# Kernel tuning notes

Hardware: AMD Instinct MI355X
Metric: run time of the kernel (lower is better)

Reference implementation:

```python
import jax, jax.numpy as jnp
import numpy as np

N_USERS = 4096
N_ITEMS = 4096
D = 64
L = 2
B = 4096
N = N_USERS + N_ITEMS


def setup_inputs() -> dict:
    key = jax.random.key(0)
    ks = jax.random.split(key, 24)
    g = lambda i, shape: jax.random.normal(ks[i], shape, dtype=jnp.float32) * 0.05
    # sparse-ish 0/1 adjacency (module calls adj.to_dense(); ~16 neighbors/node)
    adj = (jax.random.uniform(ks[0], (N, N), dtype=jnp.float32) < 0.002).astype(jnp.float32)
    users = jax.random.randint(ks[1], (B,), 0, N_USERS)
    pos_items = jax.random.randint(ks[2], (B,), 0, N_ITEMS)
    neg_items = jax.random.randint(ks[3], (B,), 0, N_ITEMS)
    return {
        "adj_matrix": adj,
        "users": users,
        "pos_items": pos_items,
        "neg_items": neg_items,
        "user_table": g(4, (N_USERS, D)),
        "item_table": g(5, (N_ITEMS, D)),
        "gcn_W": g(6, (L, D, D)), "gcn_b": g(7, (L, D)),
        "gat_W": g(8, (L, D, D)), "gat_b": g(9, (L, D)),
        "attn_W": g(10, (L, 2 * D)), "attn_b": g(11, (L,)),
        "fuse_W": g(12, (L, 2 * D, D)), "fuse_b": g(13, (L, D)),
        "actor_W": g(14, (D, D)), "actor_b": g(15, (D,)),
        "critic_W1": g(16, (2 * D, D)), "critic_b1": g(17, (D,)),
        "critic_W2": g(18, (D, 1)), "critic_b2": g(19, (1,)),
        "layer_weights": jnp.ones((L,), dtype=jnp.float32),
    }


def _leaky(x):
    return jnp.where(x >= 0, x, 0.01 * x)  # F.leaky_relu default slope


def reference(adj_matrix, users, pos_items, neg_items, user_table, item_table,
              gcn_W, gcn_b, gat_W, gat_b, attn_W, attn_b, fuse_W, fuse_b,
              actor_W, actor_b, critic_W1, critic_b1, critic_W2, critic_b2,
              layer_weights):
    all_emb = jnp.concatenate([user_table, item_table], axis=0)  # [N, D]

    # GCN stack: spmm(adj, x) then linear, relu
    gcn = [all_emb]
    for l in range(L):
        h = adj_matrix @ gcn[-1]
        gcn.append(jax.nn.relu(h @ gcn_W[l] + gcn_b[l]))

    # GAT stack: e[i,j] = leaky_relu(a1.h_i + a2.h_j + b); multiply-mask by adj, row softmax
    gat = [all_emb]
    for l in range(L):
        h = gat[-1] @ gat_W[l] + gat_b[l]  # [N, D]
        a1, a2 = attn_W[l, :D], attn_W[l, D:]
        e = _leaky((h @ a1)[:, None] + (h @ a2)[None, :] + attn_b[l])  # [N, N]
        attn = jax.nn.softmax(e * adj_matrix, axis=1)  # faithful: multiply-mask, not -inf
        gat.append(jax.nn.relu(attn @ h))

    lw = jax.nn.softmax(layer_weights)
    fused = jnp.zeros((N, D), dtype=all_emb.dtype)
    for i in range(L):
        cat = jnp.concatenate([gcn[i + 1], gat[i + 1]], axis=1)  # [N, 2D]
        fused = fused + lw[i] * jax.nn.relu(cat @ fuse_W[i] + fuse_b[i])

    user_emb, item_emb = fused[:N_USERS], fused[N_USERS:]
    u = user_emb[users]
    p = item_emb[pos_items]
    n = item_emb[neg_items]

    uf = u @ actor_W + actor_b  # Actor
    pos_score = jnp.sum(uf * p, axis=1)
    neg_score = jnp.sum(uf * n, axis=1)

    def critic(a, b):
        x = jnp.concatenate([a, b], axis=1)
        hidden = jax.nn.relu(x @ critic_W1 + critic_b1)
        return hidden @ critic_W2 + critic_b2

    return pos_score, neg_score, critic(u, p), critic(u, n)
```

## Files before the change

### kernel.cpp

```cpp
#include <hip/hip_runtime.h>

#define NTOT 8192
#define NU 4096
#define D 64
#define MAXN 64
#define ND (NTOT*D)

typedef float f4 __attribute__((ext_vector_type(4)));

__device__ __forceinline__ float wsum(float x){
  #pragma unroll
  for(int o=32;o;o>>=1) x += __shfl_xor(x,o);
  return x;
}
__device__ __forceinline__ float wmax(float x){
  #pragma unroll
  for(int o=32;o;o>>=1) x = fmaxf(x,__shfl_xor(x,o));
  return x;
}
__device__ __forceinline__ float bcastf(float x, int k){
  return __uint_as_float(__builtin_amdgcn_readlane(__float_as_uint(x),(unsigned)k));
}
__device__ __forceinline__ int bcasti(int x, int k){
  return (int)__builtin_amdgcn_readlane((unsigned)x,(unsigned)k);
}

__global__ __launch_bounds__(256) void kA(const float* __restrict__ adj,
    const float* __restrict__ ut, const float* __restrict__ it,
    const float* __restrict__ gat_W, const float* __restrict__ gat_b,
    const float* __restrict__ attn_W,
    float* __restrict__ all_emb, float* __restrict__ h0,
    float* __restrict__ q0v, float* __restrict__ k0v, float* __restrict__ S0,
    int* __restrict__ ell, int* __restrict__ nnz){
  __shared__ float Ws[D*D];
  __shared__ float red[4][D];
  int tid = threadIdx.x, lane = tid & 63, wid = tid >> 6;
  int row = blockIdx.x*4 + wid;
  for(int i = tid; i < D*D; i += 256) Ws[i] = gat_W[i];

  float x = (row < NU) ? ut[row*D + lane] : it[(row-NU)*D + lane];
  all_emb[row*D + lane] = x;

  const f4* arow = (const f4*)(adj + (size_t)row * NTOT);
  unsigned nibs[4] = {0u,0u,0u,0u};
  #pragma unroll 4
  for(int ch = 0; ch < 32; ++ch){
    f4 v = arow[ch*64 + lane];
    unsigned nib = (v.x!=0.f?1u:0u) | (v.y!=0.f?2u:0u) | (v.z!=0.f?4u:0u) | (v.w!=0.f?8u:0u);
    nibs[ch>>3] |= nib << ((ch&7)*4);
  }

  int base = 0;
  #pragma unroll
  for(int g = 0; g < 4; ++g){
    unsigned ng = nibs[g];
    for(int s = 0; s < 8; ++s){
      unsigned nib = (ng >> (s*4)) & 0xFu;
      if(__ballot(nib != 0u) == 0ull) continue;
      int ch = g*8 + s;
      #pragma unroll
      for(int j = 0; j < 4; ++j){
        unsigned long long m = __ballot(((nib>>j)&1u) != 0u);
        if(m){
          if((nib>>j)&1u){
            int below = __builtin_amdgcn_mbcnt_hi((unsigned)(m>>32),
                        __builtin_amdgcn_mbcnt_lo((unsigned)m, 0u));
            int slot = base + below;
            if(slot < MAXN) ell[row*MAXN + slot] = (ch*64 + lane)*4 + j;
          }
          base += __popcll(m);
        }
      }
    }
  }
  int cnt = base > MAXN ? MAXN : base;
  if(lane == 0) nnz[row] = cnt;

  __syncthreads();
  float h = gat_b[lane];
  #pragma unroll 16
  for(int k = 0; k < D; ++k) h = fmaf(bcastf(x, k), Ws[k*D + lane], h);
  h0[row*D + lane] = h;
  float q  = wsum(h * attn_W[lane]);
  float kk = wsum(h * attn_W[D + lane]);
  if(lane == 0){ q0v[row] = q; k0v[row] = kk; }
  red[wid][lane] = h;
  __syncthreads();
  if(wid == 0)
    atomicAdd(&S0[lane], red[0][lane] + red[1][lane] + red[2][lane] + red[3][lane]);
}

__global__ __launch_bounds__(256) void kB(
    const float* __restrict__ all_emb, const float* __restrict__ h0,
    const float* __restrict__ q0v, const float* __restrict__ k0v, const float* __restrict__ S0,
    const int* __restrict__ ell, const int* __restrict__ nnz,
    const float* __restrict__ gcn_W, const float* __restrict__ gcn_b,
    const float* __restrict__ gat_W, const float* __restrict__ gat_b,
    const float* __restrict__ attn_W, const float* __restrict__ attn_b,
    const float* __restrict__ fuse_W, const float* __restrict__ fuse_b,
    const float* __restrict__ layer_w,
    float* __restrict__ gcn1, float* __restrict__ fusedb, float* __restrict__ h1,
    float* __restrict__ q1v, float* __restrict__ k1v, float* __restrict__ S1){
  __shared__ float Ws[D*D];
  __shared__ float red[4][D];
  int tid = threadIdx.x, lane = tid & 63, wid = tid >> 6;
  int row = blockIdx.x*4 + wid;
  int cnt = nnz[row];
  int mycol = ell[row*MAXN + lane];

  for(int i = tid; i < D*D; i += 256) Ws[i] = gcn_W[i];

  float q  = q0v[row];
  float ab = attn_b[0];
  int colg = (lane < cnt) ? mycol : 0;
  float e = -1e30f;
  if(lane < cnt){
    float xx = q + k0v[colg] + ab;
    e = (xx >= 0.f) ? xx : 0.01f * xx;
  }
  float m  = fmaxf(0.f, wmax(e));
  float w  = (lane < cnt) ? expf(e - m) : 0.f;
  float em = expf(-m);
  float Z  = (float)(NTOT - cnt) * em + wsum(w);

  float accg = 0.f, acca = 0.f, hs = 0.f;
  int tt = 0;
  for(; tt + 4 <= cnt; tt += 4){
    int c0 = bcasti(mycol, tt),   c1 = bcasti(mycol, tt+1);
    int c2 = bcasti(mycol, tt+2), c3 = bcasti(mycol, tt+3);
    float w0 = bcastf(w, tt),   w1 = bcastf(w, tt+1);
    float w2 = bcastf(w, tt+2), w3 = bcastf(w, tt+3);
    float e0 = all_emb[c0*D + lane], e1 = all_emb[c1*D + lane];
    float e2 = all_emb[c2*D + lane], e3 = all_emb[c3*D + lane];
    float h0v = h0[c0*D + lane], h1v = h0[c1*D + lane];
    float h2v = h0[c2*D + lane], h3v = h0[c3*D + lane];
    accg += (e0 + e1) + (e2 + e3);
    acca = fmaf(w0, h0v, fmaf(w1, h1v, fmaf(w2, h2v, fmaf(w3, h3v, acca))));
    hs   += (h0v + h1v) + (h2v + h3v);
  }
  for(; tt < cnt; ++tt){
    int   c  = bcasti(mycol, tt);
    float wt = bcastf(w, tt);
    float ev = all_emb[c*D + lane];
    float hv = h0[c*D + lane];
    accg += ev;
    acca  = fmaf(wt, hv, acca);
    hs   += hv;
  }
  float g1 = fmaxf((acca + em*(S0[lane] - hs)) / Z, 0.f);

  __syncthreads();
  float yg = gcn_b[lane];
  #pragma unroll 16
  for(int k = 0; k < D; ++k) yg = fmaf(bcastf(accg, k), Ws[k*D + lane], yg);
  float gc1 = fmaxf(yg, 0.f);
  gcn1[row*D + lane] = gc1;
  __syncthreads();

  float l0 = layer_w[0], l1 = layer_w[1];
  float mx = fmaxf(l0, l1);
  float ex0 = expf(l0 - mx), ex1 = expf(l1 - mx);
  float lw0 = ex0 / (ex0 + ex1);
  for(int i = tid; i < D*D; i += 256) Ws[i] = fuse_W[i];
  __syncthreads();
  float y = fuse_b[lane];
  #pragma unroll 16
  for(int k = 0; k < D; ++k) y = fmaf(bcastf(gc1, k), Ws[k*D + lane], y);
  __syncthreads();
  for(int i = tid; i < D*D; i += 256) Ws[i] = fuse_W[D*D + i];
  __syncthreads();
  #pragma unroll 16
  for(int k = 0; k < D; ++k) y = fmaf(bcastf(g1, k), Ws[k*D + lane], y);
  fusedb[row*D + lane] = lw0 * fmaxf(y, 0.f);
  __syncthreads();

  for(int i = tid; i < D*D; i += 256) Ws[i] = gat_W[D*D + i];
  __syncthreads();
  float h = gat_b[D + lane];
  #pragma unroll 16
  for(int k = 0; k < D; ++k) h = fmaf(bcastf(g1, k), Ws[k*D + lane], h);
  h1[row*D + lane] = h;
  float qq = wsum(h * attn_W[2*D + lane]);
  float kk = wsum(h * attn_W[3*D + lane]);
  if(lane == 0){ q1v[row] = qq; k1v[row] = kk; }
  red[wid][lane] = h;
  __syncthreads();
  if(wid == 0)
    atomicAdd(&S1[lane], red[0][lane] + red[1][lane] + red[2][lane] + red[3][lane]);
}

__global__ __launch_bounds__(256) void kC(
    const int* __restrict__ ell, const int* __restrict__ nnz,
    const float* __restrict__ gcn1, const float* __restrict__ h1,
    const float* __restrict__ q1v, const float* __restrict__ k1v, const float* __restrict__ S1,
    const float* __restrict__ gcn_W, const float* __restrict__ gcn_b,
    const float* __restrict__ attn_b,
    const float* __restrict__ fuse_W, const float* __restrict__ fuse_b,
    const float* __restrict__ layer_w,
    float* __restrict__ fusedb){
  __shared__ float Ws[D*D];
  int tid = threadIdx.x, lane = tid & 63, wid = tid >> 6;
  int row = blockIdx.x*4 + wid;
  int cnt = nnz[row];
  int mycol = ell[row*MAXN + lane];

  for(int i = tid; i < D*D; i += 256) Ws[i] = gcn_W[D*D + i];

  float q  = q1v[row];
  float ab = attn_b[1];
  int colg = (lane < cnt) ? mycol : 0;
  float e = -1e30f;
  if(lane < cnt){
    float xx = q + k1v[colg] + ab;
    e = (xx >= 0.f) ? xx : 0.01f * xx;
  }
  float m  = fmaxf(0.f, wmax(e));
  float w  = (lane < cnt) ? expf(e - m) : 0.f;
  float em = expf(-m);
  float Z  = (float)(NTOT - cnt) * em + wsum(w);

  float accg = 0.f, acca = 0.f, hs = 0.f;
  int tt = 0;
  for(; tt + 4 <= cnt; tt += 4){
    int c0 = bcasti(mycol, tt),   c1 = bcasti(mycol, tt+1);
    int c2 = bcasti(mycol, tt+2), c3 = bcasti(mycol, tt+3);
    float w0 = bcastf(w, tt),   w1 = bcastf(w, tt+1);
    float w2 = bcastf(w, tt+2), w3 = bcastf(w, tt+3);
    float g0 = gcn1[c0*D + lane], g1_ = gcn1[c1*D + lane];
    float g2_ = gcn1[c2*D + lane], g3 = gcn1[c3*D + lane];
    float h0v = h1[c0*D + lane], h1v = h1[c1*D + lane];
    float h2v = h1[c2*D + lane], h3v = h1[c3*D + lane];
    accg += (g0 + g1_) + (g2_ + g3);
    acca = fmaf(w0, h0v, fmaf(w1, h1v, fmaf(w2, h2v, fmaf(w3, h3v, acca))));
    hs   += (h0v + h1v) + (h2v + h3v);
  }
  for(; tt < cnt; ++tt){
    int   c  = bcasti(mycol, tt);
    float wt = bcastf(w, tt);
    float gv = gcn1[c*D + lane];
    float hv = h1[c*D + lane];
    accg += gv;
    acca  = fmaf(wt, hv, acca);
    hs   += hv;
  }
  float g2 = fmaxf((acca + em*(S1[lane] - hs)) / Z, 0.f);

  __syncthreads();
  float yg = gcn_b[D + lane];
  #pragma unroll 16
  for(int k = 0; k < D; ++k) yg = fmaf(bcastf(accg, k), Ws[k*D + lane], yg);
  float gc2 = fmaxf(yg, 0.f);
  __syncthreads();

  float l0 = layer_w[0], l1 = layer_w[1];
  float mx = fmaxf(l0, l1);
  float ex0 = expf(l0 - mx), ex1 = expf(l1 - mx);
  float lw1 = ex1 / (ex0 + ex1);
  for(int i = tid; i < D*D; i += 256) Ws[i] = fuse_W[2*D*D + i];
  __syncthreads();
  float y = fuse_b[D + lane];
  #pragma unroll 16
  for(int k = 0; k < D; ++k) y = fmaf(bcastf(gc2, k), Ws[k*D + lane], y);
  __syncthreads();
  for(int i = tid; i < D*D; i += 256) Ws[i] = fuse_W[3*D*D + i];
  __syncthreads();
  #pragma unroll 16
  for(int k = 0; k < D; ++k) y = fmaf(bcastf(g2, k), Ws[k*D + lane], y);
  fusedb[row*D + lane] += lw1 * fmaxf(y, 0.f);
}

__global__ __launch_bounds__(256) void kD(const float* __restrict__ fused,
    const int* __restrict__ users, const int* __restrict__ pos, const int* __restrict__ neg,
    const float* __restrict__ AW, const float* __restrict__ abias,
    const float* __restrict__ cW1, const float* __restrict__ cb1,
    const float* __restrict__ cW2, const float* __restrict__ cb2,
    float* __restrict__ out){
  __shared__ float AWs[D*D];
  __shared__ float C1s[2*D*D];
  __shared__ float abs_[D], cb1s[D], C2s[D];
  int tid = threadIdx.x;
  for(int i = tid; i < D*D; i += 256) AWs[i] = AW[i];
  for(int i = tid; i < 2*D*D; i += 256) C1s[i] = cW1[i];
  if(tid < D){
    abs_[tid] = abias[tid];
    cb1s[tid] = cb1[tid];
    C2s[tid]  = cW2[tid];
  }
  __syncthreads();
  int lane = tid & 63;
  int bi   = blockIdx.x*4 + (tid >> 6);
  int ui = users[bi], pi = pos[bi] + NU, ni = neg[bi] + NU;
  float ud = fused[ui*D + lane], pd = fused[pi*D + lane], nd = fused[ni*D + lane];
  float ufd = abs_[lane];
  #pragma unroll 16
  for(int k = 0; k < D; ++k) ufd = fmaf(bcastf(ud, k), AWs[k*D + lane], ufd);
  float ps = wsum(ufd * pd);
  float ns = wsum(ufd * nd);
  float hu = cb1s[lane];
  #pragma unroll 16
  for(int k = 0; k < D; ++k) hu = fmaf(bcastf(ud, k), C1s[k*D + lane], hu);
  float hp = hu, hn = hu;
  #pragma unroll 16
  for(int k = 0; k < D; ++k){
    float pk = bcastf(pd, k), nk = bcastf(nd, k);
    hp = fmaf(pk, C1s[(D+k)*D + lane], hp);
    hn = fmaf(nk, C1s[(D+k)*D + lane], hn);
  }
  hp = fmaxf(hp, 0.f); hn = fmaxf(hn, 0.f);
  float cp = wsum(hp * C2s[lane]);
  float cn = wsum(hn * C2s[lane]);
  if(lane == 0){
    out[bi]         = ps;
    out[4096  + bi] = ns;
    out[8192  + bi] = cp + cb2[0];
    out[12288 + bi] = cn + cb2[0];
  }
}

extern "C" void kernel_launch(void* const* d_in, const int* in_sizes, int n_in,
                              void* d_out, int out_size, void* d_ws, size_t ws_size,
                              hipStream_t stream){
  const float* adj        = (const float*)d_in[0];
  const int*   users      = (const int*)d_in[1];
  const int*   pos        = (const int*)d_in[2];
  const int*   neg        = (const int*)d_in[3];
  const float* user_table = (const float*)d_in[4];
  const float* item_table = (const float*)d_in[5];
  const float* gcn_W      = (const float*)d_in[6];
  const float* gcn_b      = (const float*)d_in[7];
  const float* gat_W      = (const float*)d_in[8];
  const float* gat_b      = (const float*)d_in[9];
  const float* attn_W     = (const float*)d_in[10];
  const float* attn_b     = (const float*)d_in[11];
  const float* fuse_W     = (const float*)d_in[12];
  const float* fuse_b     = (const float*)d_in[13];
  const float* actor_W    = (const float*)d_in[14];
  const float* actor_b    = (const float*)d_in[15];
  const float* cW1        = (const float*)d_in[16];
  const float* cb1        = (const float*)d_in[17];
  const float* cW2        = (const float*)d_in[18];
  const float* cb2        = (const float*)d_in[19];
  const float* layer_w    = (const float*)d_in[20];

  float* ws      = (float*)d_ws;
  float* all_emb = ws;
  float* h0      = all_emb + ND;
  float* h1      = h0 + ND;
  float* gcn1    = h1 + ND;
  float* fusedb  = gcn1 + ND;
  float* q0v     = fusedb + ND;
  float* k0v     = q0v + NTOT;
  float* q1v     = k0v + NTOT;
  float* k1v     = q1v + NTOT;
  float* S0      = k1v + NTOT;
  float* S1      = S0 + D;
  int*   nnz     = (int*)(S1 + D);
  int*   ell     = nnz + NTOT;

  hipMemsetAsync(S0, 0, 2*D*sizeof(float), stream);
  kA<<<NTOT/4, 256, 0, stream>>>(adj, user_table, item_table, gat_W, gat_b, attn_W,
                                 all_emb, h0, q0v, k0v, S0, ell, nnz);
  kB<<<NTOT/4, 256, 0, stream>>>(all_emb, h0, q0v, k0v, S0, ell, nnz,
                                 gcn_W, gcn_b, gat_W, gat_b, attn_W, attn_b,
                                 fuse_W, fuse_b, layer_w,
                                 gcn1, fusedb, h1, q1v, k1v, S1);
  kC<<<NTOT/4, 256, 0, stream>>>(ell, nnz, gcn1, h1, q1v, k1v, S1,
                                 gcn_W, gcn_b, attn_b, fuse_W, fuse_b, layer_w,
                                 fusedb);
  kD<<<1024, 256, 0, stream>>>(fusedb, users, pos, neg, actor_W, actor_b,
                               cW1, cb1, cW2, cb2, (float*)d_out);
}
```

Baseline: 199.4 us.

## Split adjacency scan into separate kernel with one block per row

```diff
diff --git a/kernel.cpp b/kernel.cpp
--- a/kernel.cpp
+++ b/kernel.cpp
@@ -25,57 +25,69 @@
   return (int)__builtin_amdgcn_readlane((unsigned)x,(unsigned)k);
 }
 
-__global__ __launch_bounds__(256) void kA(const float* __restrict__ adj,
-    const float* __restrict__ ut, const float* __restrict__ it,
+__global__ __launch_bounds__(256) void kScan(const float* __restrict__ adj,
+                                             int* __restrict__ ell, int* __restrict__ nnz){
+  __shared__ int cbuf[4][MAXN];
+  __shared__ int wcnt[4];
+  int tid = threadIdx.x, lane = tid & 63, wid = tid >> 6;
+  int row = blockIdx.x;
+  const f4* arow = (const f4*)(adj + (size_t)row * NTOT);
+
+  unsigned nibsw = 0u;
+  #pragma unroll
+  for(int ch = 0; ch < 8; ++ch){
+    f4 v = arow[ch*256 + tid];
+    unsigned nib = (v.x!=0.f?1u:0u) | (v.y!=0.f?2u:0u) | (v.z!=0.f?4u:0u) | (v.w!=0.f?8u:0u);
+    nibsw |= nib << (ch*4);
+  }
+
+  int base = 0;
+  #pragma unroll
+  for(int ch = 0; ch < 8; ++ch){
+    unsigned nib = (nibsw >> (ch*4)) & 0xFu;
+    if(__ballot(nib != 0u) == 0ull) continue;
+    int f4idx = ch*256 + wid*64;
+    #pragma unroll
+    for(int j = 0; j < 4; ++j){
+      unsigned long long m = __ballot(((nib>>j)&1u) != 0u);
+      if(m){
+        if((nib>>j)&1u){
+          int below = __builtin_amdgcn_mbcnt_hi((unsigned)(m>>32),
+                      __builtin_amdgcn_mbcnt_lo((unsigned)m, 0u));
+          int slot = base + below;
+          if(slot < MAXN) cbuf[wid][slot] = (f4idx + lane)*4 + j;
+        }
+        base += __popcll(m);
+      }
+    }
+  }
+  if(lane == 0) wcnt[wid] = base < MAXN ? base : MAXN;
+  __syncthreads();
+
+  int w0 = wcnt[0], w1 = wcnt[1], w2 = wcnt[2], w3 = wcnt[3];
+  int off = (wid > 0 ? w0 : 0) + (wid > 1 ? w1 : 0) + (wid > 2 ? w2 : 0);
+  int total = w0 + w1 + w2 + w3;
+  int cnt = total < MAXN ? total : MAXN;
+  if(tid == 0) nnz[row] = cnt;
+  int mycnt = wcnt[wid];
+  if(lane < mycnt){
+    int slot = off + lane;
+    if(slot < MAXN) ell[row*MAXN + slot] = cbuf[wid][lane];
+  }
+}
+
+__global__ __launch_bounds__(256) void kEmb(const float* __restrict__ ut, const float* __restrict__ it,
     const float* __restrict__ gat_W, const float* __restrict__ gat_b,
     const float* __restrict__ attn_W,
     float* __restrict__ all_emb, float* __restrict__ h0,
-    float* __restrict__ q0v, float* __restrict__ k0v, float* __restrict__ S0,
-    int* __restrict__ ell, int* __restrict__ nnz){
+    float* __restrict__ q0v, float* __restrict__ k0v, float* __restrict__ S0){
   __shared__ float Ws[D*D];
   __shared__ float red[4][D];
   int tid = threadIdx.x, lane = tid & 63, wid = tid >> 6;
+  for(int i = tid; i < D*D; i += 256) Ws[i] = gat_W[i];
   int row = blockIdx.x*4 + wid;
-  for(int i = tid; i < D*D; i += 256) Ws[i] = gat_W[i];
-
   float x = (row < NU) ? ut[row*D + lane] : it[(row-NU)*D + lane];
   all_emb[row*D + lane] = x;
-
-  const f4* arow = (const f4*)(adj + (size_t)row * NTOT);
-  unsigned nibs[4] = {0u,0u,0u,0u};
-  #pragma unroll 4
-  for(int ch = 0; ch < 32; ++ch){
-    f4 v = arow[ch*64 + lane];
-    unsigned nib = (v.x!=0.f?1u:0u) | (v.y!=0.f?2u:0u) | (v.z!=0.f?4u:0u) | (v.w!=0.f?8u:0u);
-    nibs[ch>>3] |= nib << ((ch&7)*4);
-  }
-
-  int base = 0;
-  #pragma unroll
-  for(int g = 0; g < 4; ++g){
-    unsigned ng = nibs[g];
-    for(int s = 0; s < 8; ++s){
-      unsigned nib = (ng >> (s*4)) & 0xFu;
-      if(__ballot(nib != 0u) == 0ull) continue;
-      int ch = g*8 + s;
-      #pragma unroll
-      for(int j = 0; j < 4; ++j){
-        unsigned long long m = __ballot(((nib>>j)&1u) != 0u);
-        if(m){
-          if((nib>>j)&1u){
-            int below = __builtin_amdgcn_mbcnt_hi((unsigned)(m>>32),
-                        __builtin_amdgcn_mbcnt_lo((unsigned)m, 0u));
-            int slot = base + below;
-            if(slot < MAXN) ell[row*MAXN + slot] = (ch*64 + lane)*4 + j;
-          }
-          base += __popcll(m);
-        }
-      }
-    }
-  }
-  int cnt = base > MAXN ? MAXN : base;
-  if(lane == 0) nnz[row] = cnt;
-
   __syncthreads();
   float h = gat_b[lane];
   #pragma unroll 16
@@ -358,8 +370,9 @@
   int*   ell     = nnz + NTOT;
 
   hipMemsetAsync(S0, 0, 2*D*sizeof(float), stream);
-  kA<<<NTOT/4, 256, 0, stream>>>(adj, user_table, item_table, gat_W, gat_b, attn_W,
-                                 all_emb, h0, q0v, k0v, S0, ell, nnz);
+  kScan<<<NTOT, 256, 0, stream>>>(adj, ell, nnz);
+  kEmb<<<NTOT/4, 256, 0, stream>>>(user_table, item_table, gat_W, gat_b, attn_W,
+                                   all_emb, h0, q0v, k0v, S0);
   kB<<<NTOT/4, 256, 0, stream>>>(all_emb, h0, q0v, k0v, S0, ell, nnz,
                                  gcn_W, gcn_b, gat_W, gat_b, attn_W, attn_b,
                                  fuse_W, fuse_b, layer_w,
```

Result: slower. 216.1 us (+8.3%).
